# Kernel tuning notes

Hardware: AMD Instinct MI355X
Metric: run time of the kernel (lower is better)

The kernel has to match this reference:

```python
import jax, jax.numpy as jnp
import numpy as np

N, E = 50000, 800000
IN_DIM, HID, HEADS, OUT_DIM, NUM_CLASSES = 512, 128, 4, 64, 4


def setup_inputs() -> dict:
    key = jax.random.key(0)
    ks = jax.random.split(key, 18)
    g = lambda k, shape, s=0.05: (jax.random.normal(k, shape, dtype=jnp.float32) * s)
    x = jax.random.normal(ks[0], (N, IN_DIM), dtype=jnp.float32)
    edge_index = jax.random.randint(ks[1], (2, E), 0, N, dtype=jnp.int32)
    return {
        "x": x,
        "edge_index": edge_index,
        # GATConv layer 1 (heads=4, concat)
        "W1": g(ks[2], (IN_DIM, HEADS * HID)),
        "att_src1": g(ks[3], (HEADS, HID)),
        "att_dst1": g(ks[4], (HEADS, HID)),
        "b1": jnp.zeros((HEADS * HID,), jnp.float32),
        # GATConv layer 2 (heads=1, no concat)
        "W2": g(ks[5], (HEADS * HID, OUT_DIM)),
        "att_src2": g(ks[6], (1, OUT_DIM)),
        "att_dst2": g(ks[7], (1, OUT_DIM)),
        "b2": jnp.zeros((OUT_DIM,), jnp.float32),
        # intra_attention MLP: Linear(out,out) -> tanh -> Linear(out,1) -> softmax(dim=0)
        "Wa": g(ks[8], (OUT_DIM, OUT_DIM)),
        "ba": jnp.zeros((OUT_DIM,), jnp.float32),
        "wv": g(ks[9], (OUT_DIM, 1)),
        "bv": jnp.zeros((1,), jnp.float32),
        "class_attn": g(ks[10], (NUM_CLASSES, OUT_DIM), 0.3),
        # classifier
        "Wc": g(ks[11], (OUT_DIM, NUM_CLASSES)),
        "bc": jnp.zeros((NUM_CLASSES,), jnp.float32),
    }


def _gat_layer(x, src, dst, W, att_src, att_dst, heads, feat):
    """PyG GATConv: gather -> LeakyReLU score -> segment softmax -> scatter add."""
    n = x.shape[0]
    h = (x @ W).reshape(n, heads, feat)                     # [N,H,F]
    a_s = jnp.sum(h * att_src[None], axis=-1)               # [N,H]
    a_d = jnp.sum(h * att_dst[None], axis=-1)               # [N,H]
    e = jax.nn.leaky_relu(a_s[src] + a_d[dst], 0.2)         # [E,H]
    m = jax.ops.segment_max(e, dst, num_segments=n)         # per-dst max
    ex = jnp.exp(e - m[dst])
    s = jax.ops.segment_sum(ex, dst, num_segments=n)
    alpha = ex / (s[dst] + 1e-16)                           # [E,H]
    msg = h[src] * alpha[:, :, None]                        # [E,H,F]
    return jax.ops.segment_sum(msg, dst, num_segments=n)    # [N,H,F]


def reference(x, edge_index, W1, att_src1, att_dst1, b1, W2, att_src2, att_dst2,
              b2, Wa, ba, wv, bv, class_attn, Wc, bc):
    n = x.shape[0]
    loop = jnp.arange(n, dtype=edge_index.dtype)
    src = jnp.concatenate([edge_index[0], loop])            # add_self_loops=True
    dst = jnp.concatenate([edge_index[1], loop])

    h1 = _gat_layer(x, src, dst, W1, att_src1, att_dst1, HEADS, HID)
    h1 = h1.reshape(n, HEADS * HID) + b1                    # concat heads + bias
    h1 = jax.nn.elu(h1)

    h2 = _gat_layer(h1, src, dst, W2, att_src2, att_dst2, 1, OUT_DIM)
    h2 = h2.reshape(n, OUT_DIM) + b2                        # heads=1, concat=False

    # intra-sample attention, softmax over nodes (dim=0)
    scores = jnp.tanh(h2 @ Wa + ba) @ wv + bv               # [N,1]
    attw = jax.nn.softmax(scores, axis=0)
    xw = h2 * attw                                          # [N,OUT]

    xn = xw / jnp.maximum(jnp.linalg.norm(xw, axis=1, keepdims=True), 1e-12)
    cn = class_attn / jnp.maximum(
        jnp.linalg.norm(class_attn, axis=1, keepdims=True), 1e-12)
    inter_class_scores = xn @ cn.T                          # [N,C]

    out = xw @ Wc + bc                                      # [N,C]
    return out, xw, inter_class_scores
```

## Files before the change

### kernel.cpp

```cpp
#include <hip/hip_runtime.h>
#include <cstdint>
#include <cstddef>

typedef __attribute__((ext_vector_type(8))) short bf16x8;
typedef __attribute__((ext_vector_type(4))) float f32x4;
typedef __attribute__((ext_vector_type(8))) unsigned short u16x8;

__device__ __forceinline__ float lrelu02(float x) { return x > 0.f ? x : 0.2f * x; }
__device__ __forceinline__ unsigned short f2bf(float f) {
  unsigned u = __float_as_uint(f);
  unsigned r = u + 0x7FFFu + ((u >> 16) & 1u);
  return (unsigned short)(r >> 16);
}
__device__ __forceinline__ float bf2f(unsigned short b) {
  return __uint_as_float(((unsigned)b) << 16);
}

__device__ __forceinline__ void gll16(const void* g, void* l) {
  __builtin_amdgcn_global_load_lds(
      (const __attribute__((address_space(1))) void*)g,
      (__attribute__((address_space(3))) void*)l, 16, 0, 0);
}

__global__ void hist_k(const int* __restrict__ ei, int E, int N, int* __restrict__ counts) {
  int i = blockIdx.x * 256 + threadIdx.x;
  int Eall = E + N;
  if (i >= Eall) return;
  int dst = (i < E) ? ei[E + i] : (i - E);
  atomicAdd(&counts[dst], 1);
}

__global__ __launch_bounds__(256) void scan1_k(const int* __restrict__ counts,
                                               int* __restrict__ incl,
                                               int* __restrict__ bsum, int N) {
  int b = blockIdx.x, tid = threadIdx.x;
  int lane = tid & 63, wv = tid >> 6;
  int i = b * 256 + tid;
  int v = (i < N) ? counts[i] : 0;
#pragma unroll
  for (int o = 1; o < 64; o <<= 1) {
    int t = __shfl_up(v, o, 64);
    if (lane >= o) v += t;
  }
  __shared__ int wsum[4];
  if (lane == 63) wsum[wv] = v;
  __syncthreads();
  int base = 0;
  for (int wj = 0; wj < wv; wj++) base += wsum[wj];
  v += base;
  if (i < N) incl[i] = v;
  if (tid == 255) bsum[b] = v;
}

__global__ __launch_bounds__(256) void scan2_k(const int* __restrict__ bsum,
                                               int* __restrict__ pb, int nb) {
  int tid = threadIdx.x;
  int lane = tid & 63, wv = tid >> 6;
  int v = (tid < nb) ? bsum[tid] : 0;
  int orig = v;
#pragma unroll
  for (int o = 1; o < 64; o <<= 1) {
    int t = __shfl_up(v, o, 64);
    if (lane >= o) v += t;
  }
  __shared__ int wsum[4];
  if (lane == 63) wsum[wv] = v;
  __syncthreads();
  int base = 0;
  for (int wj = 0; wj < wv; wj++) base += wsum[wj];
  if (tid < nb) pb[tid] = v + base - orig;
}

__global__ void scan3_k(const int* __restrict__ incl, const int* __restrict__ pb,
                        int* __restrict__ offs, int* __restrict__ cursor, int N) {
  int i = blockIdx.x * 256 + threadIdx.x;
  if (i == 0) { offs[0] = 0; cursor[0] = 0; }
  if (i < N) {
    int v = incl[i] + pb[i >> 8];
    offs[i + 1] = v;
    if (i + 1 < N) cursor[i + 1] = v;
  }
}

__global__ void scatter_k(const int* __restrict__ ei, int E, int N,
                          int* __restrict__ cursor, int* __restrict__ ssrc) {
  int i = blockIdx.x * 256 + threadIdx.x;
  int Eall = E + N;
  if (i >= Eall) return;
  int src, dst;
  if (i < E) { src = ei[i]; dst = ei[E + i]; }
  else       { src = i - E; dst = i - E; }
  int pos = atomicAdd(&cursor[dst], 1);
  ssrc[pos] = src;
}

__global__ void prep_k(const float* __restrict__ W1, unsigned short* __restrict__ W1t,
                       const float* __restrict__ W2, unsigned short* __restrict__ W2t,
                       const float* __restrict__ ca, float* __restrict__ cn,
                       unsigned* __restrict__ red) {
  const int b = blockIdx.x;
  const int tid = threadIdx.x;
  const int NB1 = 1024;
  const int NB2 = 128;
  if (b < NB1) {
    int i = b * 256 + tid;
    int c = i >> 9, k = i & 511;
    W1t[i] = f2bf(W1[(size_t)k * 512 + c]);
  } else if (b < NB1 + NB2) {
    int i = (b - NB1) * 256 + tid;
    int c = i >> 9, k = i & 511;
    W2t[i] = f2bf(W2[(size_t)k * 64 + c]);
  } else {
    int lane = tid & 63, c = tid >> 6;
    float v = ca[c * 64 + lane];
    float p = v * v;
#pragma unroll
    for (int o = 32; o; o >>= 1) p += __shfl_xor(p, o);
    cn[c * 64 + lane] = v / fmaxf(sqrtf(p), 1e-12f);
    if (tid == 0) { red[0] = 0u; red[1] = 0u; }
  }
}

__global__ __launch_bounds__(512, 1) void gemm1_k(const float* __restrict__ X,
                                                  const unsigned short* __restrict__ Bt,
                                                  unsigned short* __restrict__ C,
                                                  const float* __restrict__ att_s,
                                                  const float* __restrict__ att_d,
                                                  float* __restrict__ as_out,
                                                  float* __restrict__ ad_out,
                                                  int M, int K, int Nc) {
  __shared__ unsigned short As[128][64];
  __shared__ unsigned short Bs[512][64];
  __shared__ float s_ds[4][128];
  __shared__ float s_dd[4][128];
  const int tid = threadIdx.x;
  const int lane = tid & 63;
  const int w = tid >> 6;
  const int wr = w >> 2, wc = w & 3;
  const int l16 = lane & 15, lk = lane >> 4;
  const int row0 = blockIdx.x * 128;

  f32x4 acc[4][8];
#pragma unroll
  for (int m = 0; m < 4; m++)
#pragma unroll
    for (int n = 0; n < 8; n++) acc[m][n] = (f32x4)0.f;

  const char* Bbase = (const char*)Bt;

  for (int k0 = 0; k0 < K; k0 += 64) {
#pragma unroll
    for (int i = 0; i < 8; i++) {
      int cb = i * 512 + tid;
      int c = cb >> 3, b = (cb & 7) * 16;
      gll16(Bbase + ((size_t)c * K + k0) * 2 + b, (char*)&Bs[0][0] + cb * 16);
    }
#pragma unroll
    for (int i = 0; i < 2; i++) {
      int id = i * 512 + tid;
      int r = id >> 3, c = (id & 7) * 8;
      int row = row0 + r;
      if (row >= M) row = M - 1;
      const float* src = X + (size_t)row * K + k0 + c;
      float4 a0 = *(const float4*)src;
      float4 a1 = *(const float4*)(src + 4);
      u16x8 pk;
      pk[0] = f2bf(a0.x); pk[1] = f2bf(a0.y); pk[2] = f2bf(a0.z); pk[3] = f2bf(a0.w);
      pk[4] = f2bf(a1.x); pk[5] = f2bf(a1.y); pk[6] = f2bf(a1.z); pk[7] = f2bf(a1.w);
      *(u16x8*)&As[r][c] = pk;
    }
    __syncthreads();
#pragma unroll
    for (int ks = 0; ks < 2; ks++) {
      bf16x8 af[4], bfr[8];
#pragma unroll
      for (int m = 0; m < 4; m++)
        af[m] = *(const bf16x8*)&As[wr * 64 + m * 16 + l16][ks * 32 + lk * 8];
#pragma unroll
      for (int n = 0; n < 8; n++)
        bfr[n] = *(const bf16x8*)&Bs[wc * 128 + n * 16 + l16][ks * 32 + lk * 8];
#pragma unroll
      for (int m = 0; m < 4; m++)
#pragma unroll
        for (int n = 0; n < 8; n++)
          acc[m][n] = __builtin_amdgcn_mfma_f32_16x16x32_bf16(af[m], bfr[n], acc[m][n], 0, 0, 0);
    }
    __syncthreads();
  }
#pragma unroll
  for (int m = 0; m < 4; m++) {
    int row_b = row0 + wr * 64 + m * 16 + lk * 4;
#pragma unroll
    for (int r = 0; r < 4; r++) {
      int row = row_b + r;
      if (row < M) {
#pragma unroll
        for (int n = 0; n < 8; n++) {
          int col = wc * 128 + n * 16 + l16;
          C[(size_t)row * Nc + col] = f2bf(acc[m][n][r]);
        }
      }
    }
  }
  float as_c[8], ad_c[8];
#pragma unroll
  for (int n = 0; n < 8; n++) {
    int col = wc * 128 + n * 16 + l16;
    as_c[n] = att_s[col];
    ad_c[n] = att_d[col];
  }
#pragma unroll
  for (int m = 0; m < 4; m++) {
#pragma unroll
    for (int r = 0; r < 4; r++) {
      float ps = 0.f, pd = 0.f;
#pragma unroll
      for (int n = 0; n < 8; n++) {
        ps += acc[m][n][r] * as_c[n];
        pd += acc[m][n][r] * ad_c[n];
      }
#pragma unroll
      for (int o = 8; o; o >>= 1) { ps += __shfl_xor(ps, o); pd += __shfl_xor(pd, o); }
      if (l16 == 0) {
        int rr = wr * 64 + m * 16 + lk * 4 + r;
        s_ds[wc][rr] = ps;
        s_dd[wc][rr] = pd;
      }
    }
  }
  __syncthreads();
  if (tid < 128) {
    int row = row0 + tid;
    if (row < M) {
#pragma unroll
      for (int h = 0; h < 4; h++) {
        as_out[(size_t)row * 4 + h] = s_ds[h][tid];
        ad_out[(size_t)row * 4 + h] = s_dd[h][tid];
      }
    }
  }
}

__global__ __launch_bounds__(256) void gemm2_k(const unsigned short* __restrict__ A,
                                               const unsigned short* __restrict__ Bt,
                                               unsigned short* __restrict__ C,
                                               const float* __restrict__ att_s,
                                               const float* __restrict__ att_d,
                                               float* __restrict__ as_out,
                                               float* __restrict__ ad_out,
                                               int M, int K, int Nc) {
  __shared__ unsigned short As[64][64];
  __shared__ unsigned short Bs[64][64];
  __shared__ float s_ds[2][64];
  __shared__ float s_dd[2][64];
  const int tid = threadIdx.x;
  const int lane = tid & 63;
  const int w = tid >> 6;
  const int wr = w >> 1, wc = w & 1;
  const int l16 = lane & 15, lk = lane >> 4;
  const int row0 = blockIdx.x * 64;

  f32x4 acc[2][2];
#pragma unroll
  for (int m = 0; m < 2; m++)
#pragma unroll
    for (int n = 0; n < 2; n++) acc[m][n] = (f32x4)0.f;

  const char* Abase = (const char*)A;
  const char* Bbase = (const char*)Bt;

  for (int k0 = 0; k0 < K; k0 += 64) {
#pragma unroll
    for (int i = 0; i < 2; i++) {
      int ca = i * 256 + tid;
      int r = ca >> 3, b = (ca & 7) * 16;
      gll16(Abase + ((size_t)(row0 + r) * K + k0) * 2 + b, (char*)&As[0][0] + ca * 16);
    }
#pragma unroll
    for (int i = 0; i < 2; i++) {
      int cb = i * 256 + tid;
      int c = cb >> 3, b = (cb & 7) * 16;
      gll16(Bbase + ((size_t)c * K + k0) * 2 + b, (char*)&Bs[0][0] + cb * 16);
    }
    __syncthreads();
#pragma unroll
    for (int ks = 0; ks < 2; ks++) {
      bf16x8 af[2], bfr[2];
#pragma unroll
      for (int m = 0; m < 2; m++)
        af[m] = *(const bf16x8*)&As[wr * 32 + m * 16 + l16][ks * 32 + lk * 8];
#pragma unroll
      for (int n = 0; n < 2; n++)
        bfr[n] = *(const bf16x8*)&Bs[wc * 32 + n * 16 + l16][ks * 32 + lk * 8];
#pragma unroll
      for (int m = 0; m < 2; m++)
#pragma unroll
        for (int n = 0; n < 2; n++)
          acc[m][n] = __builtin_amdgcn_mfma_f32_16x16x32_bf16(af[m], bfr[n], acc[m][n], 0, 0, 0);
    }
    __syncthreads();
  }
#pragma unroll
  for (int m = 0; m < 2; m++) {
    int row_b = row0 + wr * 32 + m * 16 + lk * 4;
#pragma unroll
    for (int r = 0; r < 4; r++) {
      int row = row_b + r;
      if (row < M) {
#pragma unroll
        for (int n = 0; n < 2; n++) {
          int col = wc * 32 + n * 16 + l16;
          C[(size_t)row * Nc + col] = f2bf(acc[m][n][r]);
        }
      }
    }
  }
  float as_c[2], ad_c[2];
#pragma unroll
  for (int n = 0; n < 2; n++) {
    int col = wc * 32 + n * 16 + l16;
    as_c[n] = att_s[col];
    ad_c[n] = att_d[col];
  }
#pragma unroll
  for (int m = 0; m < 2; m++) {
#pragma unroll
    for (int r = 0; r < 4; r++) {
      float ps = 0.f, pd = 0.f;
#pragma unroll
      for (int n = 0; n < 2; n++) {
        ps += acc[m][n][r] * as_c[n];
        pd += acc[m][n][r] * ad_c[n];
      }
#pragma unroll
      for (int o = 8; o; o >>= 1) { ps += __shfl_xor(ps, o); pd += __shfl_xor(pd, o); }
      if (l16 == 0) {
        int rr = wr * 32 + m * 16 + lk * 4 + r;
        s_ds[wc][rr] = ps;
        s_dd[wc][rr] = pd;
      }
    }
  }
  __syncthreads();
  if (tid < 64) {
    int row = row0 + tid;
    if (row < M) {
      as_out[row] = s_ds[0][tid] + s_ds[1][tid];
      ad_out[row] = s_dd[0][tid] + s_dd[1][tid];
    }
  }
}

__global__ __launch_bounds__(256) void gat_agg1_k(const unsigned short* __restrict__ hfeat,
                                                  const float* __restrict__ a_s,
                                                  const float* __restrict__ a_d,
                                                  const int* __restrict__ offs,
                                                  const int* __restrict__ ssrc,
                                                  const float* __restrict__ b1,
                                                  unsigned short* __restrict__ h1b, int N) {
  const int tid = threadIdx.x;
  const int lane = tid & 63, wave = tid >> 6;
  const int n = blockIdx.x * 4 + wave;
  if (n >= N) return;
  __shared__ int   s_src[4][64];
  __shared__ float s_ex[4][64][4];
  const int start = offs[n], end = offs[n + 1];
  const int hhl = lane >> 4;
  const float4 adv4 = *(const float4*)(a_d + (size_t)n * 4);
  const float4* as4 = (const float4*)a_s;

  float m0 = -1e30f, m1 = -1e30f, m2 = -1e30f, m3 = -1e30f;
  float S0 = 0.f, S1 = 0.f, S2 = 0.f, S3 = 0.f;
  float acc[8] = {0.f, 0.f, 0.f, 0.f, 0.f, 0.f, 0.f, 0.f};

  for (int base = start; base < end; base += 64) {
    const int cnt = min(64, end - base);
    float e0 = -1e30f, e1 = -1e30f, e2 = -1e30f, e3 = -1e30f;
    int s = 0;
    if (lane < cnt) {
      s = ssrc[base + lane];
      float4 av = as4[s];
      e0 = lrelu02(av.x + adv4.x);
      e1 = lrelu02(av.y + adv4.y);
      e2 = lrelu02(av.z + adv4.z);
      e3 = lrelu02(av.w + adv4.w);
    }
    float c0 = e0, c1 = e1, c2 = e2, c3 = e3;
#pragma unroll
    for (int o = 32; o; o >>= 1) {
      c0 = fmaxf(c0, __shfl_xor(c0, o));
      c1 = fmaxf(c1, __shfl_xor(c1, o));
      c2 = fmaxf(c2, __shfl_xor(c2, o));
      c3 = fmaxf(c3, __shfl_xor(c3, o));
    }
    float nm0 = fmaxf(m0, c0), nm1 = fmaxf(m1, c1);
    float nm2 = fmaxf(m2, c2), nm3 = fmaxf(m3, c3);
    float sc0 = __expf(m0 - nm0), sc1 = __expf(m1 - nm1);
    float sc2 = __expf(m2 - nm2), sc3 = __expf(m3 - nm3);
    m0 = nm0; m1 = nm1; m2 = nm2; m3 = nm3;
    float x0 = (lane < cnt) ? __expf(e0 - nm0) : 0.f;
    float x1 = (lane < cnt) ? __expf(e1 - nm1) : 0.f;
    float x2 = (lane < cnt) ? __expf(e2 - nm2) : 0.f;
    float x3 = (lane < cnt) ? __expf(e3 - nm3) : 0.f;
    s_src[wave][lane] = s;
    s_ex[wave][lane][0] = x0; s_ex[wave][lane][1] = x1;
    s_ex[wave][lane][2] = x2; s_ex[wave][lane][3] = x3;
#pragma unroll
    for (int o = 32; o; o >>= 1) {
      x0 += __shfl_xor(x0, o); x1 += __shfl_xor(x1, o);
      x2 += __shfl_xor(x2, o); x3 += __shfl_xor(x3, o);
    }
    S0 = S0 * sc0 + x0; S1 = S1 * sc1 + x1;
    S2 = S2 * sc2 + x2; S3 = S3 * sc3 + x3;
    float scl = (hhl == 0) ? sc0 : (hhl == 1) ? sc1 : (hhl == 2) ? sc2 : sc3;
#pragma unroll
    for (int q = 0; q < 8; q++) acc[q] *= scl;
#pragma unroll 4
    for (int j = 0; j < cnt; j++) {
      int sj = s_src[wave][j];
      float al = s_ex[wave][j][hhl];
      uint4 pk = *(const uint4*)(hfeat + ((size_t)sj << 9) + lane * 8);
      acc[0] += al * __uint_as_float(pk.x << 16);
      acc[1] += al * __uint_as_float(pk.x & 0xFFFF0000u);
      acc[2] += al * __uint_as_float(pk.y << 16);
      acc[3] += al * __uint_as_float(pk.y & 0xFFFF0000u);
      acc[4] += al * __uint_as_float(pk.z << 16);
      acc[5] += al * __uint_as_float(pk.z & 0xFFFF0000u);
      acc[6] += al * __uint_as_float(pk.w << 16);
      acc[7] += al * __uint_as_float(pk.w & 0xFFFF0000u);
    }
  }
  float inv = 1.f / (((hhl == 0) ? S0 : (hhl == 1) ? S1 : (hhl == 2) ? S2 : S3) + 1e-16f);
  const float4 b1a = *(const float4*)(b1 + lane * 8);
  const float4 b1b = *(const float4*)(b1 + lane * 8 + 4);
  float v[8];
  v[0] = acc[0] * inv + b1a.x; v[1] = acc[1] * inv + b1a.y;
  v[2] = acc[2] * inv + b1a.z; v[3] = acc[3] * inv + b1a.w;
  v[4] = acc[4] * inv + b1b.x; v[5] = acc[5] * inv + b1b.y;
  v[6] = acc[6] * inv + b1b.z; v[7] = acc[7] * inv + b1b.w;
  u16x8 outv;
#pragma unroll
  for (int q = 0; q < 8; q++) {
    float t = v[q] > 0.f ? v[q] : (__expf(v[q]) - 1.f);
    outv[q] = f2bf(t);
  }
  __builtin_nontemporal_store(outv, (u16x8*)(h1b + ((size_t)n << 9) + lane * 8));
}

__global__ __launch_bounds__(256) void gat_agg2_k(const unsigned short* __restrict__ h2b,
                                                  const float* __restrict__ a_s,
                                                  const float* __restrict__ a_d,
                                                  const int* __restrict__ offs,
                                                  const int* __restrict__ ssrc,
                                                  const float* __restrict__ b2,
                                                  const float* __restrict__ Wa,
                                                  const float* __restrict__ ba,
                                                  const float* __restrict__ wv,
                                                  const float* __restrict__ bv,
                                                  float* __restrict__ h2out,
                                                  float* __restrict__ scores, int N) {
  const int tid = threadIdx.x;
  const int lane = tid & 63, wave = tid >> 6;
  const int n = blockIdx.x * 4 + wave;
  if (n >= N) return;
  __shared__ int   s_src[4][64];
  __shared__ float s_ex[4][64];
  const int start = offs[n], end = offs[n + 1];
  const float ad = a_d[n];
  const int half = lane >> 5, l32 = lane & 31;

  float m = -1e30f, S = 0.f, acc0 = 0.f, acc1 = 0.f;
  for (int base = start; base < end; base += 64) {
    const int cnt = min(64, end - base);
    float e = -1e30f;
    int s = 0;
    if (lane < cnt) {
      s = ssrc[base + lane];
      e = lrelu02(a_s[s] + ad);
    }
    float c = e;
#pragma unroll
    for (int o = 32; o; o >>= 1) c = fmaxf(c, __shfl_xor(c, o));
    float nm = fmaxf(m, c);
    float sc = __expf(m - nm);
    m = nm;
    float x = (lane < cnt) ? __expf(e - nm) : 0.f;
    s_src[wave][lane] = s;
    s_ex[wave][lane] = x;
    float xs = x;
#pragma unroll
    for (int o = 32; o; o >>= 1) xs += __shfl_xor(xs, o);
    S = S * sc + xs;
    acc0 *= sc; acc1 *= sc;
#pragma unroll 8
    for (int j = half; j < cnt; j += 2) {
      int sj = s_src[wave][j];
      float al = s_ex[wave][j];
      unsigned pk = *(const unsigned*)(h2b + ((size_t)sj << 6) + l32 * 2);
      acc0 += al * __uint_as_float(pk << 16);
      acc1 += al * __uint_as_float(pk & 0xFFFF0000u);
    }
  }
  acc0 += __shfl_xor(acc0, 32);
  acc1 += __shfl_xor(acc1, 32);
  float inv = 1.f / (S + 1e-16f);
  float hx = acc0 * inv + b2[l32 * 2];
  float hy = acc1 * inv + b2[l32 * 2 + 1];
  if (half == 0) {
    float2 o;
    o.x = hx; o.y = hy;
    *(float2*)(h2out + ((size_t)n << 6) + l32 * 2) = o;
  }
  float t = ba[lane];
#pragma unroll 8
  for (int k = 0; k < 32; k++) {
    float a = __shfl(hx, k);
    float b = __shfl(hy, k);
    t += a * Wa[(2 * k) * 64 + lane] + b * Wa[(2 * k + 1) * 64 + lane];
  }
  t = tanhf(t);
  float p = t * wv[lane];
#pragma unroll
  for (int o = 32; o; o >>= 1) p += __shfl_xor(p, o);
  if (lane == 0) scores[n] = p + bv[0];
}

__global__ void score_sum_k(const float* __restrict__ scores, unsigned* __restrict__ red, int N) {
  int i = blockIdx.x * 256 + threadIdx.x;
  float s = (i < N) ? __expf(scores[i]) : 0.f;
#pragma unroll
  for (int o = 32; o; o >>= 1) s += __shfl_xor(s, o);
  if ((threadIdx.x & 63) == 0) atomicAdd(reinterpret_cast<float*>(red) + 1, s);
}

__global__ __launch_bounds__(256) void finalize_k(const float* __restrict__ h2,
                                                  const float* __restrict__ scores,
                                                  const unsigned* __restrict__ red,
                                                  const float* __restrict__ cn,
                                                  const float* __restrict__ Wc,
                                                  const float* __restrict__ bc,
                                                  float* __restrict__ out, int N) {
  int lane = threadIdx.x & 63, wave = threadIdx.x >> 6;
  int n = blockIdx.x * 4 + wave;
  if (n >= N) return;
  float S = __uint_as_float(red[1]);
  float attw = __expf(scores[n]) / S;
  float xw = h2[(size_t)n * 64 + lane] * attw;
  float p = xw * xw;
#pragma unroll
  for (int o = 32; o; o >>= 1) p += __shfl_xor(p, o);
  float xn = xw / fmaxf(sqrtf(p), 1e-12f);
  float i0 = xn * cn[lane],       i1 = xn * cn[64 + lane];
  float i2 = xn * cn[128 + lane], i3 = xn * cn[192 + lane];
  float o0 = xw * Wc[lane * 4 + 0], o1 = xw * Wc[lane * 4 + 1];
  float o2 = xw * Wc[lane * 4 + 2], o3 = xw * Wc[lane * 4 + 3];
#pragma unroll
  for (int o = 32; o; o >>= 1) {
    i0 += __shfl_xor(i0, o); i1 += __shfl_xor(i1, o);
    i2 += __shfl_xor(i2, o); i3 += __shfl_xor(i3, o);
    o0 += __shfl_xor(o0, o); o1 += __shfl_xor(o1, o);
    o2 += __shfl_xor(o2, o); o3 += __shfl_xor(o3, o);
  }
  float* outp   = out;
  float* xwp    = out + (size_t)N * 4;
  float* interp = out + (size_t)N * 68;
  xwp[(size_t)n * 64 + lane] = xw;
  if (lane == 0) {
    outp[n * 4 + 0] = o0 + bc[0]; outp[n * 4 + 1] = o1 + bc[1];
    outp[n * 4 + 2] = o2 + bc[2]; outp[n * 4 + 3] = o3 + bc[3];
    interp[n * 4 + 0] = i0; interp[n * 4 + 1] = i1;
    interp[n * 4 + 2] = i2; interp[n * 4 + 3] = i3;
  }
}

extern "C" void kernel_launch(void* const* d_in, const int* in_sizes, int n_in,
                              void* d_out, int out_size, void* d_ws, size_t ws_size,
                              hipStream_t stream) {
  const float* x        = (const float*)d_in[0];
  const int*   ei       = (const int*)d_in[1];
  const float* W1       = (const float*)d_in[2];
  const float* att_src1 = (const float*)d_in[3];
  const float* att_dst1 = (const float*)d_in[4];
  const float* b1       = (const float*)d_in[5];
  const float* W2       = (const float*)d_in[6];
  const float* att_src2 = (const float*)d_in[7];
  const float* att_dst2 = (const float*)d_in[8];
  const float* b2       = (const float*)d_in[9];
  const float* Wa       = (const float*)d_in[10];
  const float* ba       = (const float*)d_in[11];
  const float* wv       = (const float*)d_in[12];
  const float* bv       = (const float*)d_in[13];
  const float* class_attn = (const float*)d_in[14];
  const float* Wc       = (const float*)d_in[15];
  const float* bc       = (const float*)d_in[16];

  const int N = in_sizes[0] / 512;
  const int E = in_sizes[1] / 2;
  const int Eall = E + N;
  const int Mpad = ((N + 127) / 128) * 128;
  const int nb = (N + 255) / 256;

  char* w = (char*)d_ws;
  size_t off = 0;
  auto alloc = [&](size_t bytes) -> void* {
    off = (off + 255) & ~((size_t)255);
    void* p = w + off;
    off += bytes;
    return p;
  };
  unsigned short* h1b = (unsigned short*)alloc((size_t)Mpad * 512 * 2);
  unsigned short* hb  = (unsigned short*)alloc((size_t)N * 512 * 2);
  unsigned short* h2b = (unsigned short*)alloc((size_t)N * 64 * 2);
  float* h2     = (float*)alloc((size_t)N * 64 * 4);
  unsigned short* W1t = (unsigned short*)alloc((size_t)512 * 512 * 2);
  unsigned short* W2t = (unsigned short*)alloc((size_t)64 * 512 * 2);
  float* as1    = (float*)alloc((size_t)N * 4 * 4);
  float* ad1    = (float*)alloc((size_t)N * 4 * 4);
  float* as2    = (float*)alloc((size_t)N * 4);
  float* ad2    = (float*)alloc((size_t)N * 4);
  int*   counts = (int*)alloc((size_t)N * 4);
  int*   incl   = (int*)alloc((size_t)N * 4);
  int*   bsum   = (int*)alloc(256 * 4);
  int*   pb     = (int*)alloc(256 * 4);
  int*   offs   = (int*)alloc((size_t)(N + 1) * 4);
  int*   cursor = (int*)alloc((size_t)N * 4);
  int*   ssrc   = (int*)alloc((size_t)Eall * 4);
  float* scores = (float*)alloc((size_t)N * 4);
  unsigned* red = (unsigned*)alloc(64);
  float* cn     = (float*)alloc(256 * 4);

  const int gN256  = (N + 255) / 256;
  const int gE256  = (Eall + 255) / 256;
  const int gNode4 = (N + 3) / 4;

  hipMemsetAsync(counts, 0, (size_t)N * 4, stream);
  hist_k<<<gE256, 256, 0, stream>>>(ei, E, N, counts);
  scan1_k<<<nb, 256, 0, stream>>>(counts, incl, bsum, N);
  scan2_k<<<1, 256, 0, stream>>>(bsum, pb, nb);
  scan3_k<<<gN256, 256, 0, stream>>>(incl, pb, offs, cursor, N);
  scatter_k<<<gE256, 256, 0, stream>>>(ei, E, N, cursor, ssrc);

  prep_k<<<1024 + 128 + 1, 256, 0, stream>>>(W1, W1t, W2, W2t, class_attn, cn, red);

  gemm1_k<<<Mpad / 128, 512, 0, stream>>>(
      x, W1t, hb, att_src1, att_dst1, as1, ad1, N, 512, 512);
  gat_agg1_k<<<gNode4, 256, 0, stream>>>(hb, as1, ad1, offs, ssrc, b1, h1b, N);

  gemm2_k<<<dim3(Mpad / 64, 1), 256, 0, stream>>>(
      h1b, W2t, h2b, att_src2, att_dst2, as2, ad2, N, 512, 64);
  gat_agg2_k<<<gNode4, 256, 0, stream>>>(h2b, as2, ad2, offs, ssrc, b2,
                                         Wa, ba, wv, bv, h2, scores, N);

  score_sum_k<<<gN256, 256, 0, stream>>>(scores, red, N);
  finalize_k<<<gNode4, 256, 0, stream>>>(h2, scores, red, cn, Wc, bc,
                                         (float*)d_out, N);
}
```

Before: 424.6 us.

## Merge prep kernels, drop scan2 and score_sum, widen gemm1 to 1024 threads

```diff
diff --git a/kernel.cpp b/kernel.cpp
--- a/kernel.cpp
+++ b/kernel.cpp
@@ -22,12 +22,40 @@
       (__attribute__((address_space(3))) void*)l, 16, 0, 0);
 }
 
-__global__ void hist_k(const int* __restrict__ ei, int E, int N, int* __restrict__ counts) {
-  int i = blockIdx.x * 256 + threadIdx.x;
-  int Eall = E + N;
-  if (i >= Eall) return;
-  int dst = (i < E) ? ei[E + i] : (i - E);
-  atomicAdd(&counts[dst], 1);
+__global__ void hist_prep_k(const int* __restrict__ ei, int E, int N,
+                            int* __restrict__ counts, int gE,
+                            const float* __restrict__ W1, unsigned short* __restrict__ W1t,
+                            const float* __restrict__ W2, unsigned short* __restrict__ W2t,
+                            const float* __restrict__ ca, float* __restrict__ cn,
+                            unsigned* __restrict__ red) {
+  const int b = blockIdx.x;
+  const int tid = threadIdx.x;
+  if (b < gE) {
+    int i = b * 256 + tid;
+    int Eall = E + N;
+    if (i >= Eall) return;
+    int dst = (i < E) ? ei[E + i] : (i - E);
+    atomicAdd(&counts[dst], 1);
+  } else {
+    int bb = b - gE;
+    if (bb < 1024) {
+      int i = bb * 256 + tid;
+      int c = i >> 9, k = i & 511;
+      W1t[i] = f2bf(W1[(size_t)k * 512 + c]);
+    } else if (bb < 1024 + 128) {
+      int i = (bb - 1024) * 256 + tid;
+      int c = i >> 9, k = i & 511;
+      W2t[i] = f2bf(W2[(size_t)k * 64 + c]);
+    } else {
+      int lane = tid & 63, c = tid >> 6;
+      float v = ca[c * 64 + lane];
+      float p = v * v;
+#pragma unroll
+      for (int o = 32; o; o >>= 1) p += __shfl_xor(p, o);
+      cn[c * 64 + lane] = v / fmaxf(sqrtf(p), 1e-12f);
+      if (tid == 0) { red[0] = 0u; red[1] = 0u; }
+    }
+  }
 }
 
 __global__ __launch_bounds__(256) void scan1_k(const int* __restrict__ counts,
@@ -52,31 +80,25 @@
   if (tid == 255) bsum[b] = v;
 }
 
-__global__ __launch_bounds__(256) void scan2_k(const int* __restrict__ bsum,
-                                               int* __restrict__ pb, int nb) {
-  int tid = threadIdx.x;
-  int lane = tid & 63, wv = tid >> 6;
-  int v = (tid < nb) ? bsum[tid] : 0;
-  int orig = v;
-#pragma unroll
-  for (int o = 1; o < 64; o <<= 1) {
-    int t = __shfl_up(v, o, 64);
-    if (lane >= o) v += t;
-  }
-  __shared__ int wsum[4];
-  if (lane == 63) wsum[wv] = v;
+__global__ __launch_bounds__(256) void scan3_k(const int* __restrict__ incl,
+                                               const int* __restrict__ bsum,
+                                               int* __restrict__ offs,
+                                               int* __restrict__ cursor, int N) {
+  const int b = blockIdx.x, tid = threadIdx.x;
+  __shared__ int s_pre;
+  if (tid < 64) {
+    int p = 0;
+    for (int i = tid; i < b; i += 64) p += bsum[i];
+#pragma unroll
+    for (int o = 32; o; o >>= 1) p += __shfl_xor(p, o);
+    if (tid == 0) s_pre = p;
+  }
   __syncthreads();
-  int base = 0;
-  for (int wj = 0; wj < wv; wj++) base += wsum[wj];
-  if (tid < nb) pb[tid] = v + base - orig;
-}
-
-__global__ void scan3_k(const int* __restrict__ incl, const int* __restrict__ pb,
-                        int* __restrict__ offs, int* __restrict__ cursor, int N) {
-  int i = blockIdx.x * 256 + threadIdx.x;
+  const int prefix = s_pre;
+  int i = b * 256 + tid;
   if (i == 0) { offs[0] = 0; cursor[0] = 0; }
   if (i < N) {
-    int v = incl[i] + pb[i >> 8];
+    int v = incl[i] + prefix;
     offs[i + 1] = v;
     if (i + 1 < N) cursor[i + 1] = v;
   }
@@ -94,71 +116,42 @@
   ssrc[pos] = src;
 }
 
-__global__ void prep_k(const float* __restrict__ W1, unsigned short* __restrict__ W1t,
-                       const float* __restrict__ W2, unsigned short* __restrict__ W2t,
-                       const float* __restrict__ ca, float* __restrict__ cn,
-                       unsigned* __restrict__ red) {
-  const int b = blockIdx.x;
-  const int tid = threadIdx.x;
-  const int NB1 = 1024;
-  const int NB2 = 128;
-  if (b < NB1) {
-    int i = b * 256 + tid;
-    int c = i >> 9, k = i & 511;
-    W1t[i] = f2bf(W1[(size_t)k * 512 + c]);
-  } else if (b < NB1 + NB2) {
-    int i = (b - NB1) * 256 + tid;
-    int c = i >> 9, k = i & 511;
-    W2t[i] = f2bf(W2[(size_t)k * 64 + c]);
-  } else {
-    int lane = tid & 63, c = tid >> 6;
-    float v = ca[c * 64 + lane];
-    float p = v * v;
-#pragma unroll
-    for (int o = 32; o; o >>= 1) p += __shfl_xor(p, o);
-    cn[c * 64 + lane] = v / fmaxf(sqrtf(p), 1e-12f);
-    if (tid == 0) { red[0] = 0u; red[1] = 0u; }
-  }
-}
-
-__global__ __launch_bounds__(512, 1) void gemm1_k(const float* __restrict__ X,
-                                                  const unsigned short* __restrict__ Bt,
-                                                  unsigned short* __restrict__ C,
-                                                  const float* __restrict__ att_s,
-                                                  const float* __restrict__ att_d,
-                                                  float* __restrict__ as_out,
-                                                  float* __restrict__ ad_out,
-                                                  int M, int K, int Nc) {
+__global__ __launch_bounds__(1024, 1) void gemm1_k(const float* __restrict__ X,
+                                                   const unsigned short* __restrict__ Bt,
+                                                   unsigned short* __restrict__ C,
+                                                   const float* __restrict__ att_s,
+                                                   const float* __restrict__ att_d,
+                                                   float* __restrict__ as_out,
+                                                   float* __restrict__ ad_out,
+                                                   int M, int K, int Nc) {
   __shared__ unsigned short As[128][64];
   __shared__ unsigned short Bs[512][64];
-  __shared__ float s_ds[4][128];
-  __shared__ float s_dd[4][128];
+  __shared__ float s_ds[8][128];
+  __shared__ float s_dd[8][128];
   const int tid = threadIdx.x;
   const int lane = tid & 63;
   const int w = tid >> 6;
-  const int wr = w >> 2, wc = w & 3;
+  const int wr = w >> 3, wc = w & 7;
   const int l16 = lane & 15, lk = lane >> 4;
   const int row0 = blockIdx.x * 128;
 
-  f32x4 acc[4][8];
+  f32x4 acc[4][4];
 #pragma unroll
   for (int m = 0; m < 4; m++)
 #pragma unroll
-    for (int n = 0; n < 8; n++) acc[m][n] = (f32x4)0.f;
+    for (int n = 0; n < 4; n++) acc[m][n] = (f32x4)0.f;
 
   const char* Bbase = (const char*)Bt;
 
   for (int k0 = 0; k0 < K; k0 += 64) {
 #pragma unroll
-    for (int i = 0; i < 8; i++) {
-      int cb = i * 512 + tid;
+    for (int i = 0; i < 4; i++) {
+      int cb = i * 1024 + tid;
       int c = cb >> 3, b = (cb & 7) * 16;
       gll16(Bbase + ((size_t)c * K + k0) * 2 + b, (char*)&Bs[0][0] + cb * 16);
     }
-#pragma unroll
-    for (int i = 0; i < 2; i++) {
-      int id = i * 512 + tid;
-      int r = id >> 3, c = (id & 7) * 8;
+    {
+      int r = tid >> 3, c = (tid & 7) * 8;
       int row = row0 + r;
       if (row >= M) row = M - 1;
       const float* src = X + (size_t)row * K + k0 + c;
@@ -172,17 +165,17 @@
     __syncthreads();
 #pragma unroll
     for (int ks = 0; ks < 2; ks++) {
-      bf16x8 af[4], bfr[8];
+      bf16x8 af[4], bfr[4];
 #pragma unroll
       for (int m = 0; m < 4; m++)
         af[m] = *(const bf16x8*)&As[wr * 64 + m * 16 + l16][ks * 32 + lk * 8];
 #pragma unroll
-      for (int n = 0; n < 8; n++)
-        bfr[n] = *(const bf16x8*)&Bs[wc * 128 + n * 16 + l16][ks * 32 + lk * 8];
+      for (int n = 0; n < 4; n++)
+        bfr[n] = *(const bf16x8*)&Bs[wc * 64 + n * 16 + l16][ks * 32 + lk * 8];
 #pragma unroll
       for (int m = 0; m < 4; m++)
 #pragma unroll
-        for (int n = 0; n < 8; n++)
+        for (int n = 0; n < 4; n++)
           acc[m][n] = __builtin_amdgcn_mfma_f32_16x16x32_bf16(af[m], bfr[n], acc[m][n], 0, 0, 0);
     }
     __syncthreads();
@@ -195,17 +188,17 @@
       int row = row_b + r;
       if (row < M) {
 #pragma unroll
-        for (int n = 0; n < 8; n++) {
-          int col = wc * 128 + n * 16 + l16;
+        for (int n = 0; n < 4; n++) {
+          int col = wc * 64 + n * 16 + l16;
           C[(size_t)row * Nc + col] = f2bf(acc[m][n][r]);
         }
       }
     }
   }
-  float as_c[8], ad_c[8];
-#pragma unroll
-  for (int n = 0; n < 8; n++) {
-    int col = wc * 128 + n * 16 + l16;
+  float as_c[4], ad_c[4];
+#pragma unroll
+  for (int n = 0; n < 4; n++) {
+    int col = wc * 64 + n * 16 + l16;
     as_c[n] = att_s[col];
     ad_c[n] = att_d[col];
   }
@@ -215,7 +208,7 @@
     for (int r = 0; r < 4; r++) {
       float ps = 0.f, pd = 0.f;
 #pragma unroll
-      for (int n = 0; n < 8; n++) {
+      for (int n = 0; n < 4; n++) {
         ps += acc[m][n][r] * as_c[n];
         pd += acc[m][n][r] * ad_c[n];
       }
@@ -234,8 +227,8 @@
     if (row < M) {
 #pragma unroll
       for (int h = 0; h < 4; h++) {
-        as_out[(size_t)row * 4 + h] = s_ds[h][tid];
-        ad_out[(size_t)row * 4 + h] = s_dd[h][tid];
+        as_out[(size_t)row * 4 + h] = s_ds[2 * h][tid] + s_ds[2 * h + 1][tid];
+        ad_out[(size_t)row * 4 + h] = s_dd[2 * h][tid] + s_dd[2 * h + 1][tid];
       }
     }
   }
@@ -458,7 +451,8 @@
                                                   const float* __restrict__ wv,
                                                   const float* __restrict__ bv,
                                                   float* __restrict__ h2out,
-                                                  float* __restrict__ scores, int N) {
+                                                  float* __restrict__ scores,
+                                                  unsigned* __restrict__ red, int N) {
   const int tid = threadIdx.x;
   const int lane = tid & 63, wave = tid >> 6;
   const int n = blockIdx.x * 4 + wave;
@@ -522,15 +516,11 @@
   float p = t * wv[lane];
 #pragma unroll
   for (int o = 32; o; o >>= 1) p += __shfl_xor(p, o);
-  if (lane == 0) scores[n] = p + bv[0];
-}
-
-__global__ void score_sum_k(const float* __restrict__ scores, unsigned* __restrict__ red, int N) {
-  int i = blockIdx.x * 256 + threadIdx.x;
-  float s = (i < N) ? __expf(scores[i]) : 0.f;
-#pragma unroll
-  for (int o = 32; o; o >>= 1) s += __shfl_xor(s, o);
-  if ((threadIdx.x & 63) == 0) atomicAdd(reinterpret_cast<float*>(red) + 1, s);
+  if (lane == 0) {
+    float sc = p + bv[0];
+    scores[n] = sc;
+    atomicAdd(reinterpret_cast<float*>(red) + 1, __expf(sc));
+  }
 }
 
 __global__ __launch_bounds__(256) void finalize_k(const float* __restrict__ h2,
@@ -621,7 +611,6 @@
   int*   counts = (int*)alloc((size_t)N * 4);
   int*   incl   = (int*)alloc((size_t)N * 4);
   int*   bsum   = (int*)alloc(256 * 4);
-  int*   pb     = (int*)alloc(256 * 4);
   int*   offs   = (int*)alloc((size_t)(N + 1) * 4);
   int*   cursor = (int*)alloc((size_t)N * 4);
   int*   ssrc   = (int*)alloc((size_t)Eall * 4);
@@ -634,24 +623,21 @@
   const int gNode4 = (N + 3) / 4;
 
   hipMemsetAsync(counts, 0, (size_t)N * 4, stream);
-  hist_k<<<gE256, 256, 0, stream>>>(ei, E, N, counts);
+  hist_prep_k<<<gE256 + 1024 + 128 + 1, 256, 0, stream>>>(
+      ei, E, N, counts, gE256, W1, W1t, W2, W2t, class_attn, cn, red);
   scan1_k<<<nb, 256, 0, stream>>>(counts, incl, bsum, N);
-  scan2_k<<<1, 256, 0, stream>>>(bsum, pb, nb);
-  scan3_k<<<gN256, 256, 0, stream>>>(incl, pb, offs, cursor, N);
+  scan3_k<<<gN256, 256, 0, stream>>>(incl, bsum, offs, cursor, N);
   scatter_k<<<gE256, 256, 0, stream>>>(ei, E, N, cursor, ssrc);
 
-  prep_k<<<1024 + 128 + 1, 256, 0, stream>>>(W1, W1t, W2, W2t, class_attn, cn, red);
-
-  gemm1_k<<<Mpad / 128, 512, 0, stream>>>(
+  gemm1_k<<<Mpad / 128, 1024, 0, stream>>>(
       x, W1t, hb, att_src1, att_dst1, as1, ad1, N, 512, 512);
   gat_agg1_k<<<gNode4, 256, 0, stream>>>(hb, as1, ad1, offs, ssrc, b1, h1b, N);
 
   gemm2_k<<<dim3(Mpad / 64, 1), 256, 0, stream>>>(
       h1b, W2t, h2b, att_src2, att_dst2, as2, ad2, N, 512, 64);
   gat_agg2_k<<<gNode4, 256, 0, stream>>>(h2b, as2, ad2, offs, ssrc, b2,
-                                         Wa, ba, wv, bv, h2, scores, N);
-
-  score_sum_k<<<gN256, 256, 0, stream>>>(scores, red, N);
+                                         Wa, ba, wv, bv, h2, scores, red, N);
+
   finalize_k<<<gNode4, 256, 0, stream>>>(h2, scores, red, cn, Wc, bc,
                                          (float*)d_out, N);
 }
```

Measured after the change: 995.9 us. 2.35x slower.
